# Optimization experiments

Measured on AMD Instinct MI355X. Metric: run time of the kernel, lower is better.

The kernel has to match this reference:

```python
import jax, jax.numpy as jnp
import numpy as np

NEG_SLOPE = 0.2  # PyG GATConv default leaky_relu slope
N_NODES, N_EDGES, F_IN, HID = 25000, 200000, 64, 128


def gat_layer(x, src, dst, W, a_src, a_dst, b, heads, ch):
    """PyG-style GATConv (concat=True, eval mode). x:[N,Fin] -> [N,heads*ch]."""
    N = x.shape[0]
    h = (x @ W).reshape(N, heads, ch)                      # [N,H,C]
    al_s = jnp.sum(h * a_src, axis=-1)                     # [N,H]
    al_d = jnp.sum(h * a_dst, axis=-1)                     # [N,H]
    e = jax.nn.leaky_relu(al_s[src] + al_d[dst], NEG_SLOPE)  # [E,H]
    # segment softmax over incoming edges of each dst node (stable)
    e = e - jax.ops.segment_max(e, dst, num_segments=N)[dst]
    ex = jnp.exp(e)
    alpha = ex / jax.ops.segment_sum(ex, dst, num_segments=N)[dst]  # [E,H]
    out = jax.ops.segment_sum(h[src] * alpha[:, :, None], dst, num_segments=N)  # [N,H,C]
    return out.reshape(N, heads * ch) + b


def setup_inputs() -> dict:
    key = jax.random.key(0)
    ks = jax.random.split(key, 24)
    def g(k, shape, fan_in):
        return jax.random.normal(k, shape, dtype=jnp.float32) / np.sqrt(fan_in)
    inp = {
        "x": jax.random.normal(ks[0], (N_NODES, F_IN), dtype=jnp.float32),
        "edge_index": jax.random.randint(ks[1], (2, N_EDGES), 0, N_NODES, dtype=jnp.int64) if jax.config.jax_enable_x64 else jax.random.randint(ks[1], (2, N_EDGES), 0, N_NODES).astype(jnp.int32),
        "liquor_idx": jax.random.randint(ks[2], (4096,), 0, N_NODES),
        "ingredient_idx": jax.random.randint(ks[3], (4096,), 0, N_NODES),
        "W1": g(ks[4], (F_IN, 8 * HID), F_IN), "a_s1": g(ks[5], (8, HID), HID), "a_d1": g(ks[6], (8, HID), HID), "b1": jnp.zeros((8 * HID,), jnp.float32),
        "W2": g(ks[7], (8 * HID, 8 * HID), 8 * HID), "a_s2": g(ks[8], (8, HID), HID), "a_d2": g(ks[9], (8, HID), HID), "b2": jnp.zeros((8 * HID,), jnp.float32),
        "W3": g(ks[10], (8 * HID, HID), 8 * HID), "a_s3": g(ks[11], (1, HID), HID), "a_d3": g(ks[12], (1, HID), HID), "b3": jnp.zeros((HID,), jnp.float32),
        # MLP scorer: 256 -> 128 -> 64 -> 1
        "mw1": g(ks[13], (2 * HID, HID), 2 * HID), "mb1": jnp.zeros((HID,), jnp.float32),
        "mw2": g(ks[14], (HID, HID // 2), HID), "mb2": jnp.zeros((HID // 2,), jnp.float32),
        "mw3": g(ks[15], (HID // 2, 1), HID // 2), "mb3": jnp.zeros((1,), jnp.float32),
    }
    return inp


def reference(x, edge_index, liquor_idx, ingredient_idx,
              W1, a_s1, a_d1, b1, W2, a_s2, a_d2, b2, W3, a_s3, a_d3, b3,
              mw1, mb1, mw2, mb2, mw3, mb3):
    N = x.shape[0]
    loops = jnp.arange(N, dtype=edge_index.dtype)  # GATConv adds self-loops
    src = jnp.concatenate([edge_index[0], loops])
    dst = jnp.concatenate([edge_index[1], loops])
    h = jax.nn.relu(gat_layer(x, src, dst, W1, a_s1, a_d1, b1, 8, HID))
    h = jax.nn.relu(gat_layer(h, src, dst, W2, a_s2, a_d2, b2, 8, HID))
    h = gat_layer(h, src, dst, W3, a_s3, a_d3, b3, 1, HID)
    pair = jnp.concatenate([h[liquor_idx], h[ingredient_idx]], axis=-1)  # [B,256]
    z = jax.nn.relu(pair @ mw1 + mb1)
    z = jax.nn.relu(z @ mw2 + mb2)
    z = z @ mw3 + mb3
    return jax.nn.sigmoid(z).squeeze(-1)
```

## Files before the change

kernel.cpp:

```cpp
#include <hip/hip_runtime.h>
#include <math.h>

#define NEG_SLOPE 0.2f

typedef short short8 __attribute__((ext_vector_type(8)));
typedef float f32x4 __attribute__((ext_vector_type(4)));

__device__ __forceinline__ float lrelu(float x){ return x > 0.f ? x : NEG_SLOPE * x; }

__device__ __forceinline__ unsigned short f2bf(float f){
  union { float f; unsigned u; } v; v.f = f;
  unsigned r = v.u + 0x7fff + ((v.u >> 16) & 1);
  return (unsigned short)(r >> 16);
}
__device__ __forceinline__ float bf2f(unsigned short u){
  union { unsigned u; float f; } v; v.u = ((unsigned)u) << 16; return v.f;
}

__device__ __forceinline__ void gld16(const unsigned short* g, unsigned short* l){
  __builtin_amdgcn_global_load_lds(
      (const __attribute__((address_space(1))) unsigned int*)g,
      (__attribute__((address_space(3))) unsigned int*)l, 16, 0, 0);
}

#define MFMA_BF16 __builtin_amdgcn_mfma_f32_16x16x32_bf16

__global__ void k_count(const int* __restrict__ dst, int* __restrict__ cnt, int E){
  int e = blockIdx.x*blockDim.x + threadIdx.x;
  if (e < E) atomicAdd(&cnt[dst[e]], 1);
}

__global__ void k_blockscan(const int* __restrict__ cnt, int* __restrict__ row,
                            int* __restrict__ aux, int n){
  __shared__ int buf[256];
  int t = threadIdx.x;
  int base = blockIdx.x * 256;
  int v = (base + t < n) ? cnt[base + t] : 0;
  buf[t] = v;
  __syncthreads();
  #pragma unroll
  for (int off = 1; off < 256; off <<= 1){
    int u = (t >= off) ? buf[t - off] : 0;
    __syncthreads();
    buf[t] += u;
    __syncthreads();
  }
  if (base + t < n) row[base + t + 1] = buf[t];
  if (t == 255) aux[blockIdx.x] = buf[255];
  if (blockIdx.x == 0 && t == 0) row[0] = 0;
}

__global__ void k_addoff(const int* __restrict__ aux, int* __restrict__ row, int n){
  __shared__ int sbuf[256];
  int b = blockIdx.x, t = threadIdx.x;
  sbuf[t] = (t < b) ? aux[t] : 0;
  __syncthreads();
  #pragma unroll
  for (int off = 128; off >= 1; off >>= 1){
    if (t < off) sbuf[t] += sbuf[t + off];
    __syncthreads();
  }
  int i = b * 256 + t;
  if (i < n) row[i + 1] += sbuf[0];
}

__global__ void k_scatter(const int* __restrict__ src, const int* __restrict__ dst,
                          const int* __restrict__ row, int* __restrict__ cur,
                          int* __restrict__ csr, int E){
  int e = blockIdx.x*blockDim.x + threadIdx.x;
  if (e < E){
    int d = dst[e];
    int p = atomicAdd(&cur[d], 1);
    csr[row[d] + p] = src[e];
  }
}

__global__ void k_prep(const float* __restrict__ x, unsigned short* __restrict__ xb, int nx, int nxb,
                       const float* __restrict__ W1, unsigned short* __restrict__ Wt1,
                       const float* __restrict__ W2, unsigned short* __restrict__ Wt2,
                       const float* __restrict__ W3, unsigned short* __restrict__ Wt3,
                       const float* __restrict__ a_s1, const float* __restrict__ a_d1,
                       float* __restrict__ ws1){
  __shared__ float tile[32][33];
  int b = blockIdx.x, t = threadIdx.x;
  if (b < nxb){
    int i0 = b * 2048 + t * 8;
    if (i0 + 8 <= nx){
      float4 f0 = *reinterpret_cast<const float4*>(x + i0);
      float4 f1 = *reinterpret_cast<const float4*>(x + i0 + 4);
      short8 o;
      o[0]=f2bf(f0.x); o[1]=f2bf(f0.y); o[2]=f2bf(f0.z); o[3]=f2bf(f0.w);
      o[4]=f2bf(f1.x); o[5]=f2bf(f1.y); o[6]=f2bf(f1.z); o[7]=f2bf(f1.w);
      *reinterpret_cast<short8*>(xb + i0) = o;
    } else {
      for (int k = 0; k < 8 && i0 + k < nx; ++k) xb[i0 + k] = f2bf(x[i0 + k]);
    }
    return;
  }
  int bp = b - nxb;
  if (bp >= 64 + 1024 + 128){
    int k = bp - (64 + 1024 + 128);
    int h = t >> 5, lq = t & 31;
    float4 wv = *reinterpret_cast<const float4*>(&W1[(size_t)k * 1024 + h * 128 + lq * 4]);
    float4 sv = *reinterpret_cast<const float4*>(&a_s1[h * 128 + lq * 4]);
    float4 dv = *reinterpret_cast<const float4*>(&a_d1[h * 128 + lq * 4]);
    float ps = wv.x*sv.x + wv.y*sv.y + wv.z*sv.z + wv.w*sv.w;
    float pd = wv.x*dv.x + wv.y*dv.y + wv.z*dv.z + wv.w*dv.w;
    #pragma unroll
    for (int off = 16; off >= 1; off >>= 1){
      ps += __shfl_xor(ps, off);
      pd += __shfl_xor(pd, off);
    }
    if (lq == 0){ ws1[k * 16 + h] = ps; ws1[k * 16 + 8 + h] = pd; }
    return;
  }
  const float* W; unsigned short* Wt; int K, N, ti;
  if (bp < 64)            { W = W1; Wt = Wt1; K = 64;   N = 1024; ti = bp;
                            int kb = (ti & 1) * 32, nb = (ti >> 1) * 32;
                            int tx = t & 31, ty = t >> 5;
                            #pragma unroll
                            for (int i = ty; i < 32; i += 8) tile[i][tx] = W[(size_t)(kb+i)*N + nb+tx];
                            __syncthreads();
                            #pragma unroll
                            for (int i = ty; i < 32; i += 8) Wt[(size_t)(nb+i)*K + kb+tx] = f2bf(tile[tx][i]);
                            return; }
  if (bp < 64 + 1024)     { W = W2; Wt = Wt2; K = 1024; N = 1024; ti = bp - 64; }
  else                    { W = W3; Wt = Wt3; K = 1024; N = 128;  ti = bp - 64 - 1024; }
  int kb = (ti & 31) * 32, nb = (ti >> 5) * 32;
  int tx = t & 31, ty = t >> 5;
  #pragma unroll
  for (int i = ty; i < 32; i += 8) tile[i][tx] = W[(size_t)(kb+i)*N + nb+tx];
  __syncthreads();
  #pragma unroll
  for (int i = ty; i < 32; i += 8) Wt[(size_t)(nb+i)*K + kb+tx] = f2bf(tile[tx][i]);
}

__global__ void k_logits1(const unsigned short* __restrict__ xb, const float* __restrict__ ws,
                          float* __restrict__ ALS, float* __restrict__ ALD, int N){
  __shared__ unsigned short lx[32 * 64];
  __shared__ float lw[64 * 16];
  int t = threadIdx.x;
  int n0 = blockIdx.x * 32;
  int r = t >> 3, c = (t & 7) * 8;
  if (n0 + r < N)
    *reinterpret_cast<short8*>(&lx[r * 64 + c]) =
      *reinterpret_cast<const short8*>(&xb[(size_t)(n0 + r) * 64 + c]);
  else {
    short8 z = {0,0,0,0,0,0,0,0};
    *reinterpret_cast<short8*>(&lx[r * 64 + c]) = z;
  }
  *reinterpret_cast<float4*>(&lw[t * 4]) = *reinterpret_cast<const float4*>(&ws[t * 4]);
  __syncthreads();
  int nl = t >> 3, h = t & 7;
  if (n0 + nl >= N) return;
  float s = 0.f, d = 0.f;
  #pragma unroll 8
  for (int k = 0; k < 64; ++k){
    float xv = bf2f(lx[nl * 64 + k]);
    s = fmaf(xv, lw[k * 16 + h], s);
    d = fmaf(xv, lw[k * 16 + 8 + h], d);
  }
  ALS[(size_t)(n0 + nl) * 8 + h] = s;
  ALD[(size_t)(n0 + nl) * 8 + h] = d;
}

template<int HEADS>
__global__ void k_sm(const float* __restrict__ ALS, const float* __restrict__ ALD,
                     const int* __restrict__ row, const int* __restrict__ csr,
                     float* __restrict__ alpha, float* __restrict__ alps,
                     float* __restrict__ invl, int N){
  int idx = blockIdx.x * blockDim.x + threadIdx.x;
  int n = idx / HEADS, h = idx - n * HEADS;
  if (n >= N) return;
  float ald = ALD[(size_t)n * HEADS + h];
  float es = lrelu(ALS[(size_t)n * HEADS + h] + ald);
  float m = es;
  int beg = row[n], end = row[n + 1];
  for (int j = beg; j < end; ++j)
    m = fmaxf(m, lrelu(ALS[(size_t)csr[j] * HEADS + h] + ald));
  float ps = __expf(es - m);
  float l = ps;
  for (int j = beg; j < end; ++j){
    float p = __expf(lrelu(ALS[(size_t)csr[j] * HEADS + h] + ald) - m);
    alpha[(size_t)j * HEADS + h] = p;
    l += p;
  }
  alps[(size_t)n * HEADS + h] = ps;
  invl[(size_t)n * HEADS + h] = 1.f / l;
}

__global__ void k_gat_x(const unsigned short* __restrict__ xb, const float* __restrict__ alpha,
                        const float* __restrict__ alps, const float* __restrict__ invl,
                        const int* __restrict__ row, const int* __restrict__ csr,
                        unsigned short* __restrict__ G, int N){
  int t = threadIdx.x;
  int n = blockIdx.x * 4 + (t >> 6);
  if (n >= N) return;
  int lane = t & 63;
  float xv = bf2f(xb[(size_t)n * 64 + lane]);
  float4 s0 = *reinterpret_cast<const float4*>(&alps[(size_t)n * 8]);
  float4 s1 = *reinterpret_cast<const float4*>(&alps[(size_t)n * 8 + 4]);
  float acc[8] = {s0.x*xv, s0.y*xv, s0.z*xv, s0.w*xv, s1.x*xv, s1.y*xv, s1.z*xv, s1.w*xv};
  int beg = row[n], end = row[n + 1];
  for (int j = beg; j < end; ++j){
    int s = csr[j];
    float xs = bf2f(xb[(size_t)s * 64 + lane]);
    float4 a0 = *reinterpret_cast<const float4*>(&alpha[(size_t)j * 8]);
    float4 a1 = *reinterpret_cast<const float4*>(&alpha[(size_t)j * 8 + 4]);
    acc[0] = fmaf(a0.x, xs, acc[0]);
    acc[1] = fmaf(a0.y, xs, acc[1]);
    acc[2] = fmaf(a0.z, xs, acc[2]);
    acc[3] = fmaf(a0.w, xs, acc[3]);
    acc[4] = fmaf(a1.x, xs, acc[4]);
    acc[5] = fmaf(a1.y, xs, acc[5]);
    acc[6] = fmaf(a1.z, xs, acc[6]);
    acc[7] = fmaf(a1.w, xs, acc[7]);
  }
  float4 i0 = *reinterpret_cast<const float4*>(&invl[(size_t)n * 8]);
  float4 i1 = *reinterpret_cast<const float4*>(&invl[(size_t)n * 8 + 4]);
  float iv[8] = {i0.x, i0.y, i0.z, i0.w, i1.x, i1.y, i1.z, i1.w};
  #pragma unroll
  for (int h = 0; h < 8; ++h)
    G[(size_t)n * 512 + h * 64 + lane] = f2bf(acc[h] * iv[h]);
}

__global__ __launch_bounds__(256) void k_gemm_g(
    const unsigned short* __restrict__ G,
    const unsigned short* __restrict__ Bt,
    const float* __restrict__ bias,
    unsigned short* __restrict__ C,
    int M){
  __shared__ unsigned short As[128 * 32];
  __shared__ unsigned short Bs[128 * 32];
  const int nwg = gridDim.x;
  int bid = blockIdx.x;
  int swz = ((nwg & 7) == 0) ? ((bid & 7) * (nwg >> 3) + (bid >> 3)) : bid;
  const int head = swz % 8, byi = swz / 8;
  const int bm = byi * 128, bn = head * 128;
  const int tid  = threadIdx.x;
  const int lane = tid & 63, wave = tid >> 6;
  const int wr = wave >> 1, wc = wave & 1;
  const int lr = lane & 15, lk = lane >> 4;
  const int srow = wave * 16 + (lane >> 2);
  const int skc  = (lane & 3) * 8;
  int ar0 = bm + srow;      if (ar0 >= M) ar0 = M - 1;
  int ar1 = bm + srow + 64; if (ar1 >= M) ar1 = M - 1;
  const unsigned short* ga0 = G + (size_t)ar0 * 512 + head * 64 + skc;
  const unsigned short* ga1 = G + (size_t)ar1 * 512 + head * 64 + skc;
  const unsigned short* gb0 = Bt + (size_t)(bn + srow) * 64 + skc;
  const unsigned short* gb1 = Bt + (size_t)(bn + srow + 64) * 64 + skc;
  f32x4 acc[4][4] = {};
  #pragma unroll
  for (int k0 = 0; k0 < 64; k0 += 32){
    gld16(ga0 + k0, &As[(size_t)wave * 512]);
    gld16(ga1 + k0, &As[(size_t)(wave + 4) * 512]);
    gld16(gb0 + k0, &Bs[(size_t)wave * 512]);
    gld16(gb1 + k0, &Bs[(size_t)(wave + 4) * 512]);
    __syncthreads();
    short8 af[4], bg[4];
    #pragma unroll
    for (int m = 0; m < 4; ++m)
      af[m] = *reinterpret_cast<const short8*>(&As[(wr * 64 + m * 16 + lr) * 32 + lk * 8]);
    #pragma unroll
    for (int n = 0; n < 4; ++n)
      bg[n] = *reinterpret_cast<const short8*>(&Bs[(wc * 64 + n * 16 + lr) * 32 + lk * 8]);
    #pragma unroll
    for (int m = 0; m < 4; ++m)
      #pragma unroll
      for (int n = 0; n < 4; ++n)
        acc[m][n] = MFMA_BF16(af[m], bg[n], acc[m][n], 0, 0, 0);
    __syncthreads();
  }
  float bv[4];
  #pragma unroll
  for (int n = 0; n < 4; ++n) bv[n] = bias[bn + wc * 64 + n * 16 + lr];
  #pragma unroll
  for (int m = 0; m < 4; ++m){
    #pragma unroll
    for (int j = 0; j < 4; ++j){
      int rowi = bm + wr * 64 + m * 16 + lk * 4 + j;
      if (rowi < M){
        #pragma unroll
        for (int n = 0; n < 4; ++n)
          C[(size_t)rowi * 1024 + bn + wc * 64 + n * 16 + lr] = f2bf(fmaxf(acc[m][n][j] + bv[n], 0.f));
      }
    }
  }
}

template<int HEADS>
__global__ __launch_bounds__(256) void k_gemm_fused(
    const unsigned short* __restrict__ A, const unsigned short* __restrict__ Bt,
    unsigned short* __restrict__ C,
    const float* __restrict__ a_s, const float* __restrict__ a_d,
    float* __restrict__ ALS, float* __restrict__ ALD,
    int M, int N, int K, int gxc){
  __shared__ unsigned short SMEM[2 * 128 * 32];
  unsigned short* As = SMEM;
  unsigned short* Bs = SMEM + 128 * 32;
  const int nwg = gridDim.x;
  int bid = blockIdx.x;
  int swz = ((nwg & 7) == 0) ? ((bid & 7) * (nwg >> 3) + (bid >> 3)) : bid;
  const int bxi = swz % gxc, byi = swz / gxc;
  const int bm = byi * 128, bn = bxi * 128;
  const int head = bxi;
  const int tid  = threadIdx.x;
  const int lane = tid & 63, wave = tid >> 6;
  const int wr = wave >> 1, wc = wave & 1;
  const int lr = lane & 15, lk = lane >> 4;
  const int srow = wave * 16 + (lane >> 2);
  const int skc  = (lane & 3) * 8;
  int ar0 = bm + srow;      if (ar0 >= M) ar0 = M - 1;
  int ar1 = bm + srow + 64; if (ar1 >= M) ar1 = M - 1;
  const unsigned short* ga0 = A  + (size_t)ar0 * K + skc;
  const unsigned short* ga1 = A  + (size_t)ar1 * K + skc;
  const unsigned short* gb0 = Bt + (size_t)(bn + srow) * K + skc;
  const unsigned short* gb1 = Bt + (size_t)(bn + srow + 64) * K + skc;
  f32x4 acc[4][4] = {};
  for (int k0 = 0; k0 < K; k0 += 32){
    gld16(ga0 + k0, &As[(size_t)wave * 512]);
    gld16(ga1 + k0, &As[(size_t)(wave + 4) * 512]);
    gld16(gb0 + k0, &Bs[(size_t)wave * 512]);
    gld16(gb1 + k0, &Bs[(size_t)(wave + 4) * 512]);
    __syncthreads();
    short8 af[4], bg[4];
    #pragma unroll
    for (int m = 0; m < 4; ++m)
      af[m] = *reinterpret_cast<const short8*>(&As[(wr * 64 + m * 16 + lr) * 32 + lk * 8]);
    #pragma unroll
    for (int n = 0; n < 4; ++n)
      bg[n] = *reinterpret_cast<const short8*>(&Bs[(wc * 64 + n * 16 + lr) * 32 + lk * 8]);
    #pragma unroll
    for (int m = 0; m < 4; ++m)
      #pragma unroll
      for (int n = 0; n < 4; ++n)
        acc[m][n] = MFMA_BF16(af[m], bg[n], acc[m][n], 0, 0, 0);
    __syncthreads();
  }
  #pragma unroll
  for (int m = 0; m < 4; ++m){
    #pragma unroll
    for (int j = 0; j < 4; ++j){
      int rowi = bm + wr * 64 + m * 16 + lk * 4 + j;
      if (rowi < M){
        #pragma unroll
        for (int n = 0; n < 4; ++n)
          C[(size_t)rowi * N + bn + wc * 64 + n * 16 + lr] = f2bf(acc[m][n][j]);
      }
    }
  }
  float as4[4], ad4[4];
  #pragma unroll
  for (int n = 0; n < 4; ++n){
    as4[n] = a_s[head * 128 + wc * 64 + n * 16 + lr];
    ad4[n] = a_d[head * 128 + wc * 64 + n * 16 + lr];
  }
  float* red = (float*)SMEM;
  #pragma unroll
  for (int m = 0; m < 4; ++m){
    #pragma unroll
    for (int j = 0; j < 4; ++j){
      float ps = 0.f;
      #pragma unroll
      for (int n = 0; n < 4; ++n) ps = fmaf(acc[m][n][j], as4[n], ps);
      red[(wr * 64 + m * 16 + lk * 4 + j) * 32 + wc * 16 + lr] = ps;
    }
  }
  __syncthreads();
  if (tid < 128){
    float s = 0.f;
    #pragma unroll
    for (int i = 0; i < 32; ++i) s += red[tid * 32 + ((i + tid) & 31)];
    int gr = bm + tid;
    if (gr < M) ALS[(size_t)gr * HEADS + head] = s;
  }
  __syncthreads();
  #pragma unroll
  for (int m = 0; m < 4; ++m){
    #pragma unroll
    for (int j = 0; j < 4; ++j){
      float pd = 0.f;
      #pragma unroll
      for (int n = 0; n < 4; ++n) pd = fmaf(acc[m][n][j], ad4[n], pd);
      red[(wr * 64 + m * 16 + lk * 4 + j) * 32 + wc * 16 + lr] = pd;
    }
  }
  __syncthreads();
  if (tid < 128){
    float s = 0.f;
    #pragma unroll
    for (int i = 0; i < 32; ++i) s += red[tid * 32 + ((i + tid) & 31)];
    int gr = bm + tid;
    if (gr < M) ALD[(size_t)gr * HEADS + head] = s;
  }
}

__global__ __launch_bounds__(512, 2) void k_gemm256p8(
    const unsigned short* __restrict__ A,
    const unsigned short* __restrict__ Bt,
    unsigned short* __restrict__ C,
    const float* __restrict__ a_s, const float* __restrict__ a_d,
    float* __restrict__ ALS, float* __restrict__ ALD,
    int M, int N, int K, int gxc){
  __shared__ unsigned short smem[2 * 32768];
  const int nwg = gridDim.x;
  int bid = blockIdx.x;
  int swz = ((nwg & 7) == 0) ? ((bid & 7) * (nwg >> 3) + (bid >> 3)) : bid;
  const int bxi = swz % gxc, byi = swz / gxc;
  const int bm = byi * 256, bn = bxi * 256;
  const int tid = threadIdx.x;
  const int lane = tid & 63, wave = tid >> 6;
  const int wr = wave >> 2, wc = wave & 3;
  const int lr = lane & 15, lk = lane >> 4;
  const int sr = tid >> 3;
  const int scol = ((tid & 7) << 3) ^ ((sr & 7) << 3);
  unsigned offA[4], offB[4];
  #pragma unroll
  for (int u = 0; u < 4; ++u){
    int r = bm + u * 64 + sr; if (r >= M) r = M - 1;
    offA[u] = (unsigned)r * (unsigned)K + scol;
    offB[u] = (unsigned)(bn + u * 64 + sr) * (unsigned)K + scol;
  }
  const int wdst = wave * 512;
  const int NKT = K >> 6;
  const int NIT = NKT >> 1;

  #define STA(T,u) gld16(A  + (size_t)offA[u] + (size_t)(T)*64, &smem[((T)&1)*32768 + (u)*4096 + wdst])
  #define STB(T,u) gld16(Bt + (size_t)offB[u] + (size_t)(T)*64, &smem[((T)&1)*32768 + 16384 + (u)*4096 + wdst])

  #pragma unroll
  for (int u = 0; u < 4; ++u) STA(0, u);
  #pragma unroll
  for (int u = 0; u < 4; ++u) STB(0, u);
  #pragma unroll
  for (int u = 0; u < 4; ++u) STA(1, u);
  asm volatile("s_waitcnt vmcnt(4)" ::: "memory");
  __builtin_amdgcn_s_barrier();

  f32x4 acc[8][4] = {};
  short8 af[4][2], bg[4][2];

  #define RD_A(moff) \
    _Pragma("unroll") \
    for (int m = 0; m < 4; ++m){ \
      int row = wr * 128 + (m + (moff)) * 16 + lr; \
      int rb = row * 64, sw = (row & 7) << 3; \
      af[m][0] = *reinterpret_cast<const short8*>(&sa[rb + ((lk * 8) ^ sw)]); \
      af[m][1] = *reinterpret_cast<const short8*>(&sa[rb + ((32 + lk * 8) ^ sw)]); \
    }
  #define RD_B(n0_, n1_) \
    _Pragma("unroll") \
    for (int n = (n0_); n < (n1_); ++n){ \
      int row = wc * 64 + n * 16 + lr; \
      int rb = row * 64, sw = (row & 7) << 3; \
      bg[n][0] = *reinterpret_cast<const short8*>(&sb[rb + ((lk * 8) ^ sw)]); \
      bg[n][1] = *reinterpret_cast<const short8*>(&sb[rb + ((32 + lk * 8) ^ sw)]); \
    }
  #define SYNC_MFMA_BEG \
    __builtin_amdgcn_s_barrier(); \
    asm volatile("s_waitcnt lgkmcnt(0)" ::: "memory"); \
    __builtin_amdgcn_sched_barrier(0); \
    __builtin_amdgcn_s_setprio(1);
  #define QUAD(mb, nb) \
    _Pragma("unroll") \
    for (int m = 0; m < 4; ++m) \
      _Pragma("unroll") \
      for (int n = 0; n < 2; ++n){ \
        acc[(mb)+m][(nb)+n] = MFMA_BF16(af[m][0], bg[(nb)+n][0], acc[(mb)+m][(nb)+n], 0, 0, 0); \
        acc[(mb)+m][(nb)+n] = MFMA_BF16(af[m][1], bg[(nb)+n][1], acc[(mb)+m][(nb)+n], 0, 0, 0); \
      }
  #define SYNC_MFMA_END \
    __builtin_amdgcn_s_setprio(0); \
    __builtin_amdgcn_s_barrier();

  for (int it = 0; it < NIT; ++it){
    const int T = it << 1;
    {
      const unsigned short* sa = &smem[(T & 1) * 32768];
      const unsigned short* sb = sa + 16384;
      RD_A(0); RD_B(0, 2);
      STB(T + 1, 0); STB(T + 1, 1);
      SYNC_MFMA_BEG; QUAD(0, 0); SYNC_MFMA_END;
      RD_B(2, 4);
      STB(T + 1, 2); STB(T + 1, 3);
      SYNC_MFMA_BEG; QUAD(0, 2); SYNC_MFMA_END;
      RD_A(4);
      if (T + 2 < NKT){ STA(T + 2, 0); STA(T + 2, 2); }
      SYNC_MFMA_BEG; QUAD(4, 0); SYNC_MFMA_END;
      if (T + 2 < NKT){ STA(T + 2, 1); STA(T + 2, 3); }
      __builtin_amdgcn_s_barrier();
      __builtin_amdgcn_s_setprio(1);
      QUAD(4, 2);
      __builtin_amdgcn_s_setprio(0);
      asm volatile("s_waitcnt vmcnt(4)" ::: "memory");
      __builtin_amdgcn_s_barrier();
    }
    {
      const unsigned short* sa = &smem[((T + 1) & 1) * 32768];
      const unsigned short* sb = sa + 16384;
      RD_A(0); RD_B(0, 2);
      if (T + 2 < NKT){ STB(T + 2, 0); STB(T + 2, 1); }
      SYNC_MFMA_BEG; QUAD(0, 0); SYNC_MFMA_END;
      RD_B(2, 4);
      if (T + 2 < NKT){ STB(T + 2, 2); STB(T + 2, 3); }
      SYNC_MFMA_BEG; QUAD(0, 2); SYNC_MFMA_END;
      RD_A(4);
      if (T + 3 < NKT){ STA(T + 3, 0); STA(T + 3, 2); }
      SYNC_MFMA_BEG; QUAD(4, 0); SYNC_MFMA_END;
      if (T + 3 < NKT){ STA(T + 3, 1); STA(T + 3, 3); }
      __builtin_amdgcn_s_barrier();
      __builtin_amdgcn_s_setprio(1);
      QUAD(4, 2);
      __builtin_amdgcn_s_setprio(0);
      asm volatile("s_waitcnt vmcnt(4)" ::: "memory");
      __builtin_amdgcn_s_barrier();
    }
  }

  #pragma unroll
  for (int m = 0; m < 8; ++m){
    #pragma unroll
    for (int j = 0; j < 4; ++j){
      int row = bm + wr * 128 + m * 16 + lk * 4 + j;
      if (row < M){
        #pragma unroll
        for (int n = 0; n < 4; ++n)
          C[(size_t)row * N + bn + wc * 64 + n * 16 + lr] = f2bf(acc[m][n][j]);
      }
    }
  }
  const int hloc = wc >> 1;
  float as4[4], ad4[4];
  #pragma unroll
  for (int n = 0; n < 4; ++n){
    as4[n] = a_s[(bxi * 2 + hloc) * 128 + (wc & 1) * 64 + n * 16 + lr];
    ad4[n] = a_d[(bxi * 2 + hloc) * 128 + (wc & 1) * 64 + n * 16 + lr];
  }
  float2* red = (float2*)smem;
  __syncthreads();
  #pragma unroll
  for (int hh = 0; hh < 2; ++hh){
    if (hloc == hh){
      #pragma unroll
      for (int m = 0; m < 8; ++m){
        #pragma unroll
        for (int j = 0; j < 4; ++j){
          float ps = 0.f, pd = 0.f;
          #pragma unroll
          for (int n = 0; n < 4; ++n){
            ps = fmaf(acc[m][n][j], as4[n], ps);
            pd = fmaf(acc[m][n][j], ad4[n], pd);
          }
          red[(wr * 128 + m * 16 + lk * 4 + j) * 32 + (wc & 1) * 16 + lr] = make_float2(ps, pd);
        }
      }
    }
    __syncthreads();
    if (tid < 256){
      float ss = 0.f, sd = 0.f;
      #pragma unroll
      for (int i = 0; i < 32; ++i){
        float2 v = red[tid * 32 + ((i + tid) & 31)];
        ss += v.x; sd += v.y;
      }
      int gr = bm + tid;
      if (gr < M){
        ALS[(size_t)gr * 8 + bxi * 2 + hh] = ss;
        ALD[(size_t)gr * 8 + bxi * 2 + hh] = sd;
      }
    }
    __syncthreads();
  }
  #undef STA
  #undef STB
  #undef RD_A
  #undef RD_B
  #undef SYNC_MFMA_BEG
  #undef QUAD
  #undef SYNC_MFMA_END
}

__global__ void k_gat2(const unsigned short* __restrict__ hp, const float* __restrict__ alpha,
                       const float* __restrict__ alps, const float* __restrict__ invl,
                       const int* __restrict__ row, const int* __restrict__ csr,
                       const float* __restrict__ bias, unsigned short* __restrict__ outv, int N){
  int n = blockIdx.x;
  int t = threadIdx.x;
  int h = t >> 4;
  int c0 = (t & 15) * 8;
  float sp = alps[(size_t)n * 8 + h];
  const unsigned short* hpn = hp + ((size_t)n * 8 + h) * 128 + c0;
  short8 hv8 = *reinterpret_cast<const short8*>(hpn);
  float accA[8], accB[8] = {};
  #pragma unroll
  for (int v = 0; v < 8; ++v) accA[v] = sp * bf2f((unsigned short)hv8[v]);
  int beg = row[n], end = row[n + 1];
  int j = beg;
  for (; j + 1 < end; j += 2){
    int s0 = csr[j], s1 = csr[j + 1];
    float p0 = alpha[(size_t)j * 8 + h];
    float p1 = alpha[(size_t)(j + 1) * 8 + h];
    short8 v0 = *reinterpret_cast<const short8*>(hp + ((size_t)s0 * 8 + h) * 128 + c0);
    short8 v1 = *reinterpret_cast<const short8*>(hp + ((size_t)s1 * 8 + h) * 128 + c0);
    #pragma unroll
    for (int v = 0; v < 8; ++v){
      accA[v] = fmaf(p0, bf2f((unsigned short)v0[v]), accA[v]);
      accB[v] = fmaf(p1, bf2f((unsigned short)v1[v]), accB[v]);
    }
  }
  if (j < end){
    int s0 = csr[j];
    float p0 = alpha[(size_t)j * 8 + h];
    short8 v0 = *reinterpret_cast<const short8*>(hp + ((size_t)s0 * 8 + h) * 128 + c0);
    #pragma unroll
    for (int v = 0; v < 8; ++v) accA[v] = fmaf(p0, bf2f((unsigned short)v0[v]), accA[v]);
  }
  float inv = invl[(size_t)n * 8 + h];
  size_t ob = ((size_t)n * 8 + h) * 128 + c0;
  #pragma unroll
  for (int v = 0; v < 8; ++v){
    float o = fmaxf((accA[v] + accB[v]) * inv + bias[h * 128 + c0 + v], 0.f);
    outv[ob + v] = f2bf(o);
  }
}

__global__ void k_pair(const unsigned short* __restrict__ hp,
                       const float* __restrict__ al, const float* __restrict__ aldv,
                       const int* __restrict__ row, const int* __restrict__ csr,
                       const float* __restrict__ bias,
                       const int* __restrict__ liq, const int* __restrict__ ing,
                       const float* __restrict__ mw1, const float* __restrict__ mb1,
                       const float* __restrict__ mw2, const float* __restrict__ mb2,
                       const float* __restrict__ mw3, const float* __restrict__ mb3,
                       float* __restrict__ out, int B){
  __shared__ float pairv[256];
  __shared__ float z1[128];
  __shared__ float z2[64];
  int r = blockIdx.x;
  int t = threadIdx.x;
  int w = t >> 6;
  int lane = t & 63;
  int n = w ? ing[r] : liq[r];
  float ald = aldv[n];
  float es = lrelu(al[n] + ald);
  int beg = row[n], end = row[n + 1];
  float m = es;
  for (int j = beg; j < end; ++j)
    m = fmaxf(m, lrelu(al[csr[j]] + ald));
  float ps = __expf(es - m);
  float l = ps;
  int c0 = lane * 2;
  ushort2 hv = *reinterpret_cast<const ushort2*>(hp + (size_t)n * 128 + c0);
  float a0 = ps * bf2f(hv.x), a1 = ps * bf2f(hv.y);
  for (int j = beg; j < end; ++j){
    int s = csr[j];
    float p = __expf(lrelu(al[s] + ald) - m);
    ushort2 v = *reinterpret_cast<const ushort2*>(hp + (size_t)s * 128 + c0);
    a0 = fmaf(p, bf2f(v.x), a0);
    a1 = fmaf(p, bf2f(v.y), a1);
    l += p;
  }
  float inv = 1.f / l;
  pairv[w * 128 + c0]     = a0 * inv + bias[c0];
  pairv[w * 128 + c0 + 1] = a1 * inv + bias[c0 + 1];
  __syncthreads();
  float acc1 = mb1[t];
  for (int k = 0; k < 256; ++k) acc1 = fmaf(pairv[k], mw1[k * 128 + t], acc1);
  z1[t] = fmaxf(acc1, 0.f);
  __syncthreads();
  if (t < 64){
    float a2 = mb2[t];
    for (int k = 0; k < 128; ++k) a2 = fmaf(z1[k], mw2[k * 64 + t], a2);
    z2[t] = fmaxf(a2, 0.f);
  }
  __syncthreads();
  if (t < 64){
    float p = z2[t] * mw3[t];
    #pragma unroll
    for (int off = 32; off >= 1; off >>= 1) p += __shfl_xor(p, off);
    if (t == 0) out[r] = 1.f / (1.f + __expf(-(p + mb3[0])));
  }
  (void)B;
}

extern "C" void kernel_launch(void* const* d_in, const int* in_sizes, int n_in,
                              void* d_out, int out_size, void* d_ws, size_t ws_size,
                              hipStream_t stream){
  const float* x   = (const float*)d_in[0];
  const int*   ei  = (const int*)  d_in[1];
  const int*   liq = (const int*)  d_in[2];
  const int*   ing = (const int*)  d_in[3];
  const float* W1  = (const float*)d_in[4];
  const float* as1 = (const float*)d_in[5];
  const float* ad1 = (const float*)d_in[6];
  const float* b1  = (const float*)d_in[7];
  const float* W2  = (const float*)d_in[8];
  const float* as2 = (const float*)d_in[9];
  const float* ad2 = (const float*)d_in[10];
  const float* b2  = (const float*)d_in[11];
  const float* W3  = (const float*)d_in[12];
  const float* as3 = (const float*)d_in[13];
  const float* ad3 = (const float*)d_in[14];
  const float* b3  = (const float*)d_in[15];
  const float* mw1 = (const float*)d_in[16];
  const float* mb1 = (const float*)d_in[17];
  const float* mw2 = (const float*)d_in[18];
  const float* mb2 = (const float*)d_in[19];
  const float* mw3 = (const float*)d_in[20];
  const float* mb3 = (const float*)d_in[21];
  float* out = (float*)d_out;

  const int N = in_sizes[0] / 64;
  const int E = in_sizes[1] / 2;
  const int B = in_sizes[2];
  const int* srcp = ei;
  const int* dstp = ei + E;

  char* w = (char*)d_ws;
  auto alloc = [&](size_t bytes) -> char* {
    char* p = w;
    w += (bytes + 255) & ~(size_t)255;
    return p;
  };
  unsigned short* P    = (unsigned short*)alloc((size_t)N * 1024 * 2);
  unsigned short* Hb   = (unsigned short*)alloc((size_t)N * 1024 * 2);
  unsigned short* xb   = (unsigned short*)alloc((size_t)N * 64 * 2);
  unsigned short* Wt1  = (unsigned short*)alloc((size_t)1024 * 64 * 2);
  unsigned short* Wt2  = (unsigned short*)alloc((size_t)1024 * 1024 * 2);
  unsigned short* Wt3  = (unsigned short*)alloc((size_t)128 * 1024 * 2);
  float* ALS  = (float*)alloc((size_t)N * 8 * 4);
  float* ALD  = (float*)alloc((size_t)N * 8 * 4);
  float* alpha= (float*)alloc((size_t)E * 8 * 4);
  float* alps = (float*)alloc((size_t)N * 8 * 4);
  float* invl = (float*)alloc((size_t)N * 8 * 4);
  float* ws1  = (float*)alloc((size_t)64 * 16 * 4);
  int*   row  = (int*)  alloc((size_t)(N + 1) * 4);
  int*   cntcur = (int*)alloc((size_t)2 * N * 4);
  int*   cnt  = cntcur;
  int*   cur  = cntcur + N;
  int*   aux  = (int*)  alloc((size_t)256 * 4);
  int*   csr  = (int*)  alloc((size_t)E * 4);
  unsigned short* G = P;
  (void)ws_size; (void)n_in; (void)out_size;

  int nx = N * 64;
  int nxb = (nx + 2047) / 2048;
  k_prep<<<nxb + 64 + 1024 + 128 + 64, 256, 0, stream>>>(
      x, xb, nx, nxb, W1, Wt1, W2, Wt2, W3, Wt3, as1, ad1, ws1);

  hipMemsetAsync(cntcur, 0, (size_t)2 * N * 4, stream);
  int eb = (E + 255) / 256;
  int nb = (N + 255) / 256;
  k_count<<<eb, 256, 0, stream>>>(dstp, cnt, E);
  k_blockscan<<<nb, 256, 0, stream>>>(cnt, row, aux, N);
  k_addoff<<<nb, 256, 0, stream>>>(aux, row, N);
  k_scatter<<<eb, 256, 0, stream>>>(srcp, dstp, row, cur, csr, E);

  const int mt  = (N + 127) / 128;
  const int mt2 = (N + 255) / 256;
  const int smb8 = (N * 8 + 255) / 256;

  k_logits1<<<(N + 31) / 32, 256, 0, stream>>>(xb, ws1, ALS, ALD, N);
  k_sm<8><<<smb8, 256, 0, stream>>>(ALS, ALD, row, csr, alpha, alps, invl, N);
  k_gat_x<<<(N + 3) / 4, 256, 0, stream>>>(xb, alpha, alps, invl, row, csr, G, N);
  k_gemm_g<<<8 * mt, 256, 0, stream>>>(G, Wt1, b1, Hb, N);

  k_gemm256p8<<<4 * mt2, 512, 0, stream>>>(Hb, Wt2, P, as2, ad2, ALS, ALD, N, 1024, 1024, 4);
  k_sm<8><<<smb8, 256, 0, stream>>>(ALS, ALD, row, csr, alpha, alps, invl, N);
  k_gat2<<<N, 128, 0, stream>>>(P, alpha, alps, invl, row, csr, b2, Hb, N);

  k_gemm_fused<1><<<1 * mt, 256, 0, stream>>>(Hb, Wt3, P, as3, ad3, ALS, ALD, N, 128, 1024, 1);
  k_pair<<<B, 128, 0, stream>>>(P, ALS, ALD, row, csr, b3, liq, ing,
                                mw1, mb1, mw2, mb2, mw3, mb3, out, B);
}
```

Baseline: 319.8 us.

## Store layer-2 projections and attention weights head-major for per-head aggregation

The layer-2 GEMM now writes its bf16 output as [head][node][128] instead of [node][head*128], and the second softmax writes alpha as [head][edge]. A new aggregation kernel assigns each block one head and 16 nodes, so each lane group reads per-head rows and contiguous per-head alpha values. The aim is better coalescing of alpha loads and smaller per-head gather footprints, plus fewer, larger blocks than the old one-node-per-block launch. In exchange the GEMM epilogue writes a strided layout, and all heads still run at the same time, so the gather locality gain may be limited.

New measurement: 305.1 us. 4.6% less time.

```diff
diff --git a/kernel.cpp b/kernel.cpp
--- a/kernel.cpp
+++ b/kernel.cpp
@@ -164,11 +164,11 @@
   ALD[(size_t)(n0 + nl) * 8 + h] = d;
 }
 
-template<int HEADS>
+template<int HEADS, int TR>
 __global__ void k_sm(const float* __restrict__ ALS, const float* __restrict__ ALD,
                      const int* __restrict__ row, const int* __restrict__ csr,
                      float* __restrict__ alpha, float* __restrict__ alps,
-                     float* __restrict__ invl, int N){
+                     float* __restrict__ invl, int N, int E){
   int idx = blockIdx.x * blockDim.x + threadIdx.x;
   int n = idx / HEADS, h = idx - n * HEADS;
   if (n >= N) return;
@@ -182,7 +182,8 @@
   float l = ps;
   for (int j = beg; j < end; ++j){
     float p = __expf(lrelu(ALS[(size_t)csr[j] * HEADS + h] + ald) - m);
-    alpha[(size_t)j * HEADS + h] = p;
+    if (TR) alpha[(size_t)h * E + j] = p;
+    else    alpha[(size_t)j * HEADS + h] = p;
     l += p;
   }
   alps[(size_t)n * HEADS + h] = ps;
@@ -398,7 +399,7 @@
 __global__ __launch_bounds__(512, 2) void k_gemm256p8(
     const unsigned short* __restrict__ A,
     const unsigned short* __restrict__ Bt,
-    unsigned short* __restrict__ C,
+    unsigned short* __restrict__ Php,
     const float* __restrict__ a_s, const float* __restrict__ a_d,
     float* __restrict__ ALS, float* __restrict__ ALD,
     int M, int N, int K, int gxc){
@@ -517,6 +518,9 @@
     }
   }
 
+  const int hloc = wc >> 1;
+  const int head = bxi * 2 + hloc;
+  const int cc = (wc & 1) * 64;
   #pragma unroll
   for (int m = 0; m < 8; ++m){
     #pragma unroll
@@ -525,16 +529,15 @@
       if (row < M){
         #pragma unroll
         for (int n = 0; n < 4; ++n)
-          C[(size_t)row * N + bn + wc * 64 + n * 16 + lr] = f2bf(acc[m][n][j]);
+          Php[((size_t)head * M + row) * 128 + cc + n * 16 + lr] = f2bf(acc[m][n][j]);
       }
     }
   }
-  const int hloc = wc >> 1;
   float as4[4], ad4[4];
   #pragma unroll
   for (int n = 0; n < 4; ++n){
-    as4[n] = a_s[(bxi * 2 + hloc) * 128 + (wc & 1) * 64 + n * 16 + lr];
-    ad4[n] = a_d[(bxi * 2 + hloc) * 128 + (wc & 1) * 64 + n * 16 + lr];
+    as4[n] = a_s[head * 128 + cc + n * 16 + lr];
+    ad4[n] = a_d[head * 128 + cc + n * 16 + lr];
   }
   float2* red = (float2*)smem;
   __syncthreads();
@@ -580,17 +583,22 @@
   #undef SYNC_MFMA_END
 }
 
-__global__ void k_gat2(const unsigned short* __restrict__ hp, const float* __restrict__ alpha,
-                       const float* __restrict__ alps, const float* __restrict__ invl,
-                       const int* __restrict__ row, const int* __restrict__ csr,
-                       const float* __restrict__ bias, unsigned short* __restrict__ outv, int N){
-  int n = blockIdx.x;
+__global__ void k_gat2h(const unsigned short* __restrict__ Php,
+                        const float* __restrict__ alpha,
+                        const float* __restrict__ alps, const float* __restrict__ invl,
+                        const int* __restrict__ row, const int* __restrict__ csr,
+                        const float* __restrict__ bias, unsigned short* __restrict__ outv,
+                        int N, int E){
+  int h = blockIdx.x & 7;
+  int nb = blockIdx.x >> 3;
   int t = threadIdx.x;
-  int h = t >> 4;
+  int n = nb * 16 + (t >> 4);
+  if (n >= N) return;
   int c0 = (t & 15) * 8;
+  const unsigned short* hb = Php + (size_t)h * N * 128;
+  const float* alp = alpha + (size_t)h * E;
   float sp = alps[(size_t)n * 8 + h];
-  const unsigned short* hpn = hp + ((size_t)n * 8 + h) * 128 + c0;
-  short8 hv8 = *reinterpret_cast<const short8*>(hpn);
+  short8 hv8 = *reinterpret_cast<const short8*>(hb + (size_t)n * 128 + c0);
   float accA[8], accB[8] = {};
   #pragma unroll
   for (int v = 0; v < 8; ++v) accA[v] = sp * bf2f((unsigned short)hv8[v]);
@@ -598,10 +606,9 @@
   int j = beg;
   for (; j + 1 < end; j += 2){
     int s0 = csr[j], s1 = csr[j + 1];
-    float p0 = alpha[(size_t)j * 8 + h];
-    float p1 = alpha[(size_t)(j + 1) * 8 + h];
-    short8 v0 = *reinterpret_cast<const short8*>(hp + ((size_t)s0 * 8 + h) * 128 + c0);
-    short8 v1 = *reinterpret_cast<const short8*>(hp + ((size_t)s1 * 8 + h) * 128 + c0);
+    float p0 = alp[j], p1 = alp[j + 1];
+    short8 v0 = *reinterpret_cast<const short8*>(hb + (size_t)s0 * 128 + c0);
+    short8 v1 = *reinterpret_cast<const short8*>(hb + (size_t)s1 * 128 + c0);
     #pragma unroll
     for (int v = 0; v < 8; ++v){
       accA[v] = fmaf(p0, bf2f((unsigned short)v0[v]), accA[v]);
@@ -610,8 +617,8 @@
   }
   if (j < end){
     int s0 = csr[j];
-    float p0 = alpha[(size_t)j * 8 + h];
-    short8 v0 = *reinterpret_cast<const short8*>(hp + ((size_t)s0 * 8 + h) * 128 + c0);
+    float p0 = alp[j];
+    short8 v0 = *reinterpret_cast<const short8*>(hb + (size_t)s0 * 128 + c0);
     #pragma unroll
     for (int v = 0; v < 8; ++v) accA[v] = fmaf(p0, bf2f((unsigned short)v0[v]), accA[v]);
   }
@@ -761,13 +768,13 @@
   const int smb8 = (N * 8 + 255) / 256;
 
   k_logits1<<<(N + 31) / 32, 256, 0, stream>>>(xb, ws1, ALS, ALD, N);
-  k_sm<8><<<smb8, 256, 0, stream>>>(ALS, ALD, row, csr, alpha, alps, invl, N);
+  k_sm<8,0><<<smb8, 256, 0, stream>>>(ALS, ALD, row, csr, alpha, alps, invl, N, E);
   k_gat_x<<<(N + 3) / 4, 256, 0, stream>>>(xb, alpha, alps, invl, row, csr, G, N);
   k_gemm_g<<<8 * mt, 256, 0, stream>>>(G, Wt1, b1, Hb, N);
 
   k_gemm256p8<<<4 * mt2, 512, 0, stream>>>(Hb, Wt2, P, as2, ad2, ALS, ALD, N, 1024, 1024, 4);
-  k_sm<8><<<smb8, 256, 0, stream>>>(ALS, ALD, row, csr, alpha, alps, invl, N);
-  k_gat2<<<N, 128, 0, stream>>>(P, alpha, alps, invl, row, csr, b2, Hb, N);
+  k_sm<8,1><<<smb8, 256, 0, stream>>>(ALS, ALD, row, csr, alpha, alps, invl, N, E);
+  k_gat2h<<<8 * ((N + 15) / 16), 256, 0, stream>>>(P, alpha, alps, invl, row, csr, b2, Hb, N, E);
 
   k_gemm_fused<1><<<1 * mt, 256, 0, stream>>>(Hb, Wt3, P, as3, ad3, ALS, ALD, N, 128, 1024, 1);
   k_pair<<<B, 128, 0, stream>>>(P, ALS, ALD, row, csr, b3, liq, ing,
```
